# Optimization experiments

Measured on AMD Instinct MI355X. Metric: run time of the kernel, lower is better.

Reference implementation:

```python
import jax, jax.numpy as jnp
import numpy as np

H_BANDWIDTH = 0.5
EPS = 1e-5


def setup_inputs() -> dict:
    key = jax.random.key(0)
    k1, k2 = jax.random.split(key)
    x = jax.random.normal(k1, (4, 256, 64, 64), dtype=jnp.float32)
    y = jax.random.normal(k2, (4, 256, 64, 64), dtype=jnp.float32)
    return {"x": x, "y": y}


def reference(x, y):
    # x, y: (N, C, H, W), H=W=64 so no pooling branch is taken
    N, C, H, W = x.shape
    # mean over batch and spatial dims of y -> per-channel mu, shape (1, C, 1, 1)
    y_mu = jnp.mean(y, axis=(0, 2, 3)).reshape(1, C, 1, 1)
    x_c = x - y_mu
    y_c = y - y_mu
    # L2-normalize over channel dim
    x_n = x_c / jnp.linalg.norm(x_c, axis=1, keepdims=True)
    y_n = y_c / jnp.linalg.norm(y_c, axis=1, keepdims=True)
    x_n = x_n.reshape(N, C, H * W)
    y_n = y_n.reshape(N, C, H * W)
    # cosine similarity: (N, HW, HW)
    cos = jnp.einsum("ncp,ncq->npq", x_n, y_n)
    d = 1.0 - cos
    d_min = jnp.min(d, axis=2, keepdims=True)
    d_tilde = d / (d_min + EPS)
    w = jnp.exp((1.0 - d_tilde) / H_BANDWIDTH)
    cx_ij = w / jnp.sum(w, axis=2, keepdims=True)
    cx = jnp.mean(jnp.max(cx_ij, axis=1), axis=1)  # (N,)
    cx_loss = jnp.mean(-jnp.log(cx + EPS))
    return cx_loss
```

## Files before the change

### kernel.cpp

```cpp
#include <hip/hip_runtime.h>
#include <hip/hip_bf16.h>

typedef short bf16x8 __attribute__((ext_vector_type(8)));
typedef float f32x4 __attribute__((ext_vector_type(4)));

#define NB 4
#define C 256
#define HW 4096
#define NROWS (NB * HW)
#define EPSF 1e-5f

__device__ __forceinline__ unsigned short f2bf(float f) {
    unsigned int u = __float_as_uint(f);
    unsigned int r = u + 0x7fffu + ((u >> 16) & 1u);
    return (unsigned short)(r >> 16);
}
__device__ __forceinline__ float bf2f(unsigned int h) {
    return __uint_as_float(h << 16);
}
__device__ __forceinline__ void unpack8(uint4 u, float* v) {
    unsigned int w0 = u.x, w1 = u.y, w2 = u.z, w3 = u.w;
    v[0] = bf2f(w0 & 0xffffu); v[1] = bf2f(w0 >> 16);
    v[2] = bf2f(w1 & 0xffffu); v[3] = bf2f(w1 >> 16);
    v[4] = bf2f(w2 & 0xffffu); v[5] = bf2f(w2 >> 16);
    v[6] = bf2f(w3 & 0xffffu); v[7] = bf2f(w3 >> 16);
}
__device__ __forceinline__ float waveReduceSum(float v) {
    for (int off = 32; off > 0; off >>= 1) v += __shfl_xor(v, off);
    return v;
}
typedef __attribute__((address_space(1))) const unsigned int glb_cu;
typedef __attribute__((address_space(3))) unsigned int lds_u;
__device__ __forceinline__ void async_copy16(const unsigned short* g, unsigned short* l) {
    __builtin_amdgcn_global_load_lds((glb_cu*)g, (lds_u*)l, 16, 0, 0);
}

__global__ __launch_bounds__(256) void mu_kernel(const float* __restrict__ y,
                                                 float* __restrict__ mu,
                                                 float* __restrict__ cxsum,
                                                 unsigned int* __restrict__ ticket) {
    int c = blockIdx.x;
    int tid = threadIdx.x;
    if (c == 0) {
        if (tid < NB) cxsum[tid] = 0.f;
        if (tid == NB) *ticket = 0u;
    }
    float s = 0.f;
    const float* base = y + (size_t)c * HW;
    for (int n = 0; n < NB; n++) {
        const float* bn = base + (size_t)n * C * HW;
        for (int i = tid; i < HW; i += 256) s += bn[i];
    }
    s = waveReduceSum(s);
    __shared__ float red[4];
    int lane = tid & 63, wave = tid >> 6;
    if (lane == 0) red[wave] = s;
    __syncthreads();
    if (tid == 0) mu[c] = (red[0] + red[1] + red[2] + red[3]) * (1.0f / 16384.0f);
}

#define TP 32
#define TSTRIDE 257
__global__ __launch_bounds__(256) void prep_kernel(const float* __restrict__ x,
                                                   const float* __restrict__ y,
                                                   const float* __restrict__ mu,
                                                   unsigned short* __restrict__ Xn,
                                                   unsigned short* __restrict__ Yn) {
    __shared__ float smu[C];
    __shared__ float tile[TP * TSTRIDE];
    __shared__ float red[8 * 32];
    __shared__ float invn[TP];
    int tid = threadIdx.x;
    smu[tid] = mu[tid];
    int blk = blockIdx.x;
    int n = blk >> 7;
    int p0 = (blk & 127) * TP;
    int tp = tid & 31, cc = tid >> 5;
    __syncthreads();
    for (int pass = 0; pass < 2; pass++) {
        const float* in = pass ? y : x;
        unsigned short* out = pass ? Yn : Xn;
        const float* base = in + (size_t)n * C * HW + p0 + tp;
        float ssq = 0.f;
        for (int c = cc; c < C; c += 8) {
            float v = base[(size_t)c * HW] - smu[c];
            tile[tp * TSTRIDE + c] = v;
            ssq += v * v;
        }
        red[cc * 32 + tp] = ssq;
        __syncthreads();
        if (tid < 32) {
            float s = 0.f;
            for (int k = 0; k < 8; k++) s += red[k * 32 + tid];
            invn[tid] = rsqrtf(s);
        }
        __syncthreads();
        int c2 = (tid & 127) * 2;
        int pp = tid >> 7;
        for (int p = pp; p < TP; p += 2) {
            float inv = invn[p];
            unsigned short b0 = f2bf(tile[p * TSTRIDE + c2] * inv);
            unsigned short b1 = f2bf(tile[p * TSTRIDE + c2 + 1] * inv);
            unsigned int pack = (unsigned int)b0 | ((unsigned int)b1 << 16);
            ((unsigned int*)out)[(size_t)(n * HW + p0 + p) * (C / 2) + (c2 >> 1)] = pack;
        }
        __syncthreads();
    }
}

#define EPSTRIDE 136
#define STAGE(s)                                                               \
    do {                                                                       \
        unsigned short* lA = lds_us;                                           \
        unsigned short* lB = lds_us + 8192;                                    \
        _Pragma("unroll")                                                      \
        for (int t = 0; t < 4; t++) {                                          \
            int slot = t * 256 + tid;                                          \
            int r = slot >> 3, cl = slot & 7;                                  \
            int c = (s) * 8 + (cl ^ (r & 7));                                  \
            async_copy16(Ab + (size_t)r * C + c * 8, lA + slot * 8);           \
        }                                                                      \
        _Pragma("unroll")                                                      \
        for (int t = 0; t < 4; t++) {                                          \
            int slot = t * 256 + tid;                                          \
            int r = slot >> 3, cl = slot & 7;                                  \
            int c = (s) * 8 + (cl ^ (r & 7));                                  \
            async_copy16(Bb + (size_t)r * C + c * 8, lB + slot * 8);           \
        }                                                                      \
    } while (0)

#define COMPUTE()                                                              \
    do {                                                                       \
        const unsigned short* lA = lds_us;                                     \
        const unsigned short* lB = lds_us + 8192;                              \
        _Pragma("unroll")                                                      \
        for (int kkl = 0; kkl < 2; kkl++) {                                    \
            int cl4 = kkl * 4 + quad;                                          \
            int clp = cl4 ^ (mrow & 7);                                        \
            bf16x8 af[4], bfr[4];                                              \
            _Pragma("unroll")                                                  \
            for (int i = 0; i < 4; i++) {                                      \
                af[i]  = *(const bf16x8*)(lA + (wm + i * 16 + mrow) * 64 + clp * 8); \
                bfr[i] = *(const bf16x8*)(lB + (wn + i * 16 + mrow) * 64 + clp * 8); \
            }                                                                  \
            _Pragma("unroll")                                                  \
            for (int i = 0; i < 4; i++)                                        \
                _Pragma("unroll")                                              \
                for (int j = 0; j < 4; j++)                                    \
                    acc[i][j] = __builtin_amdgcn_mfma_f32_16x16x32_bf16(af[i], bfr[j], acc[i][j], 0, 0, 0); \
        }                                                                      \
    } while (0)

__global__ __launch_bounds__(256, 4) void gemm_cos(const unsigned short* __restrict__ Xn,
                                                   const unsigned short* __restrict__ Yn,
                                                   unsigned short* __restrict__ Cos) {
    __shared__ unsigned short lds_us[17408];
    int n = blockIdx.z;
    int pBase = blockIdx.y * 128, qBase = blockIdx.x * 128;
    const unsigned short* Ab = Xn + ((size_t)n * HW + pBase) * C;
    const unsigned short* Bb = Yn + ((size_t)n * HW + qBase) * C;
    int tid = threadIdx.x, lane = tid & 63, wave = tid >> 6;
    int wm = (wave >> 1) * 64, wn = (wave & 1) * 64;
    int mrow = lane & 15, quad = lane >> 4;

    f32x4 acc[4][4];
#pragma unroll
    for (int i = 0; i < 4; i++)
#pragma unroll
        for (int j = 0; j < 4; j++) acc[i][j] = (f32x4){0.f, 0.f, 0.f, 0.f};

#pragma unroll
    for (int s = 0; s < 4; s++) {
        STAGE(s);
        __syncthreads();
        COMPUTE();
        __syncthreads();
    }

    unsigned short* epb = lds_us;
    int col = lane & 15, quad4 = quad * 4;
#pragma unroll
    for (int i = 0; i < 4; i++)
#pragma unroll
        for (int j = 0; j < 4; j++)
#pragma unroll
            for (int r = 0; r < 4; r++)
                epb[(wm + i * 16 + quad4 + r) * EPSTRIDE + wn + j * 16 + col] = f2bf(acc[i][j][r]);
    __syncthreads();
    unsigned short* Crow = Cos + (size_t)n * HW * HW;
#pragma unroll
    for (int it = 0; it < 8; it++) {
        int e = it * 2048 + tid * 8;
        int r = e >> 7, cg = e & 127;
        uint4 o = *(const uint4*)(epb + r * EPSTRIDE + cg);
        *(uint4*)(Crow + (size_t)(pBase + r) * HW + qBase + cg) = o;
    }
}

__global__ __launch_bounds__(256, 3) void rowcol(const unsigned short* __restrict__ Cos,
                                                 unsigned short* __restrict__ partial) {
    int n = blockIdx.y, chunk = blockIdx.x;
    int tid = threadIdx.x, lane = tid & 63, wave = tid >> 6;
    const unsigned short* rowbase = Cos + ((size_t)n * HW + chunk * 8) * HW;
    __shared__ float redm[8][4];
    __shared__ float sval[8][4];

    uint4 d[8][2];
#pragma unroll
    for (int r = 0; r < 8; r++) {
        const unsigned short* rp = rowbase + (size_t)r * HW;
        d[r][0] = *(const uint4*)(rp + tid * 8);
        d[r][1] = *(const uint4*)(rp + 2048 + tid * 8);
    }

    float m8[8];
#pragma unroll
    for (int r = 0; r < 8; r++) {
        float v[16];
        unpack8(d[r][0], v); unpack8(d[r][1], v + 8);
        float m = v[0];
#pragma unroll
        for (int k = 1; k < 16; k++) m = fmaxf(m, v[k]);
        m8[r] = m;
    }
#pragma unroll
    for (int off = 32; off > 0; off >>= 1)
#pragma unroll
        for (int r = 0; r < 8; r++) m8[r] = fmaxf(m8[r], __shfl_xor(m8[r], off));
    if (lane == 0)
#pragma unroll
        for (int r = 0; r < 8; r++) redm[r][wave] = m8[r];
    __syncthreads();

    float alpha[8], basec[8];
#pragma unroll
    for (int r = 0; r < 8; r++) {
        float M = fmaxf(fmaxf(redm[r][0], redm[r][1]), fmaxf(redm[r][2], redm[r][3]));
        alpha[r] = 2.0f / ((1.0f - M) + EPSF);
        basec[r] = 2.0f - alpha[r];
    }

    float s8[8];
#pragma unroll
    for (int r = 0; r < 8; r++) {
        float v[16];
        unpack8(d[r][0], v); unpack8(d[r][1], v + 8);
        float s = 0.f;
#pragma unroll
        for (int k = 0; k < 16; k++) s += __expf(fmaf(alpha[r], v[k], basec[r]));
        s8[r] = s;
    }
#pragma unroll
    for (int off = 32; off > 0; off >>= 1)
#pragma unroll
        for (int r = 0; r < 8; r++) s8[r] += __shfl_xor(s8[r], off);
    if (lane == 0)
#pragma unroll
        for (int r = 0; r < 8; r++) sval[r][wave] = s8[r];
    __syncthreads();

    float cmax[16];
#pragma unroll
    for (int k = 0; k < 16; k++) cmax[k] = -1e30f;
#pragma unroll
    for (int r = 0; r < 8; r++) {
        float S = sval[r][0] + sval[r][1] + sval[r][2] + sval[r][3];
        float beta = basec[r] - __logf(S);
        float v[16];
        unpack8(d[r][0], v); unpack8(d[r][1], v + 8);
#pragma unroll
        for (int k = 0; k < 16; k++) cmax[k] = fmaxf(cmax[k], fmaf(alpha[r], v[k], beta));
    }

    unsigned short* outp = partial + ((size_t)(n * 512 + chunk)) * HW;
    uint4 o0, o1;
    o0.x = (unsigned int)f2bf(cmax[0]) | ((unsigned int)f2bf(cmax[1]) << 16);
    o0.y = (unsigned int)f2bf(cmax[2]) | ((unsigned int)f2bf(cmax[3]) << 16);
    o0.z = (unsigned int)f2bf(cmax[4]) | ((unsigned int)f2bf(cmax[5]) << 16);
    o0.w = (unsigned int)f2bf(cmax[6]) | ((unsigned int)f2bf(cmax[7]) << 16);
    o1.x = (unsigned int)f2bf(cmax[8]) | ((unsigned int)f2bf(cmax[9]) << 16);
    o1.y = (unsigned int)f2bf(cmax[10]) | ((unsigned int)f2bf(cmax[11]) << 16);
    o1.z = (unsigned int)f2bf(cmax[12]) | ((unsigned int)f2bf(cmax[13]) << 16);
    o1.w = (unsigned int)f2bf(cmax[14]) | ((unsigned int)f2bf(cmax[15]) << 16);
    *(uint4*)(outp + tid * 8) = o0;
    *(uint4*)(outp + 2048 + tid * 8) = o1;
}

__global__ __launch_bounds__(256) void colred(const unsigned short* __restrict__ partial,
                                              float* __restrict__ cxsum,
                                              unsigned int* __restrict__ ticket,
                                              float* __restrict__ out) {
    int n = blockIdx.y, g = blockIdx.x;
    int tid = threadIdx.x;
    int qo = tid & 7;
    int cs = tid >> 3;
    const unsigned short* p = partial + ((size_t)(n * 512 + cs)) * HW + g * 64 + qo * 8;
    float mx[8];
#pragma unroll
    for (int k = 0; k < 8; k++) mx[k] = -1e30f;
#pragma unroll 4
    for (int c = cs; c < 512; c += 32) {
        uint4 u = *(const uint4*)p;
        float v[8];
        unpack8(u, v);
#pragma unroll
        for (int k = 0; k < 8; k++) mx[k] = fmaxf(mx[k], v[k]);
        p += (size_t)32 * HW;
    }
    __shared__ float sm[32][64];
#pragma unroll
    for (int k = 0; k < 8; k++) sm[cs][qo * 8 + k] = mx[k];
    __syncthreads();
    if (tid < 64) {
        float mm = -1e30f;
#pragma unroll
        for (int s = 0; s < 32; s++) mm = fmaxf(mm, sm[s][tid]);
        float sv = __expf(mm);
        sv = waveReduceSum(sv);
        if (tid == 0) {
            atomicAdd(&cxsum[n], sv);
            __threadfence();
            unsigned int old = atomicAdd(ticket, 1u);
            if (old == (unsigned int)(64 * NB - 1)) {
                __threadfence();
                float loss = 0.f;
                for (int b = 0; b < NB; b++) {
                    float csn = atomicAdd(&cxsum[b], 0.0f);
                    loss += -logf(csn * (1.0f / 4096.0f) + EPSF);
                }
                out[0] = loss * 0.25f;
            }
        }
    }
}

extern "C" void kernel_launch(void* const* d_in, const int* in_sizes, int n_in,
                              void* d_out, int out_size, void* d_ws, size_t ws_size,
                              hipStream_t stream) {
    const float* x = (const float*)d_in[0];
    const float* y = (const float*)d_in[1];
    float* out = (float*)d_out;
    char* ws = (char*)d_ws;

    float* mu               = (float*)(ws + 0);
    float* cxsum            = (float*)(ws + 1024);
    unsigned int* ticket    = (unsigned int*)(ws + 1040);
    unsigned short* Xn      = (unsigned short*)(ws + 2097152);
    unsigned short* Yn      = (unsigned short*)(ws + 10485760);
    unsigned short* partial = (unsigned short*)(ws + 2097152);
    unsigned short* Cos     = (unsigned short*)(ws + 18874368);

    mu_kernel<<<C, 256, 0, stream>>>(y, mu, cxsum, ticket);
    prep_kernel<<<NROWS / TP, 256, 0, stream>>>(x, y, mu, Xn, Yn);
    gemm_cos<<<dim3(HW / 128, HW / 128, NB), 256, 0, stream>>>(Xn, Yn, Cos);
    rowcol<<<dim3(512, NB), 256, 0, stream>>>(Cos, partial);
    colred<<<dim3(64, NB), 256, 0, stream>>>(partial, cxsum, ticket, out);
}
```

Baseline: 197.0 us.

## Widen parallelism and vectorize loads in mu, prep and column-reduce kernels

The mu kernel now runs one block per (channel, batch) pair, reading with float4 loads and writing per-batch partial sums that prep_kernel combines. prep_kernel loads four spatial positions per thread with float4 instead of scalar loads, and the sum-of-squares reduction grows to 32 partials. colred launches twice as many blocks, each covering 32 columns over 64 row-slices, with the ticket threshold adjusted to match. The aim is more blocks in flight and fewer, wider memory transactions in the memory-bound auxiliary kernels, at the cost of extra partial-sum traffic and scattered LDS stores in the prep transpose.

Result: faster. 172.9 us (-12.2%).

```diff
diff --git a/kernel.cpp b/kernel.cpp
--- a/kernel.cpp
+++ b/kernel.cpp
@@ -36,62 +36,73 @@
 }
 
 __global__ __launch_bounds__(256) void mu_kernel(const float* __restrict__ y,
-                                                 float* __restrict__ mu,
+                                                 float* __restrict__ mup,
                                                  float* __restrict__ cxsum,
                                                  unsigned int* __restrict__ ticket) {
-    int c = blockIdx.x;
+    int c = blockIdx.x, n = blockIdx.y;
     int tid = threadIdx.x;
-    if (c == 0) {
+    if (c == 0 && n == 0) {
         if (tid < NB) cxsum[tid] = 0.f;
         if (tid == NB) *ticket = 0u;
     }
+    const float4* b4 = (const float4*)(y + (size_t)n * C * HW + (size_t)c * HW);
     float s = 0.f;
-    const float* base = y + (size_t)c * HW;
-    for (int n = 0; n < NB; n++) {
-        const float* bn = base + (size_t)n * C * HW;
-        for (int i = tid; i < HW; i += 256) s += bn[i];
+#pragma unroll
+    for (int k = 0; k < 4; k++) {
+        float4 v = b4[tid + k * 256];
+        s += (v.x + v.y) + (v.z + v.w);
     }
     s = waveReduceSum(s);
     __shared__ float red[4];
     int lane = tid & 63, wave = tid >> 6;
     if (lane == 0) red[wave] = s;
     __syncthreads();
-    if (tid == 0) mu[c] = (red[0] + red[1] + red[2] + red[3]) * (1.0f / 16384.0f);
+    if (tid == 0) mup[n * C + c] = (red[0] + red[1]) + (red[2] + red[3]);
 }
 
 #define TP 32
 #define TSTRIDE 257
 __global__ __launch_bounds__(256) void prep_kernel(const float* __restrict__ x,
                                                    const float* __restrict__ y,
-                                                   const float* __restrict__ mu,
+                                                   const float* __restrict__ mup,
                                                    unsigned short* __restrict__ Xn,
                                                    unsigned short* __restrict__ Yn) {
     __shared__ float smu[C];
     __shared__ float tile[TP * TSTRIDE];
-    __shared__ float red[8 * 32];
+    __shared__ float red[32 * 32];
     __shared__ float invn[TP];
     int tid = threadIdx.x;
-    smu[tid] = mu[tid];
+    smu[tid] = (mup[tid] + mup[C + tid] + mup[2 * C + tid] + mup[3 * C + tid]) * (1.0f / 16384.0f);
     int blk = blockIdx.x;
     int n = blk >> 7;
     int p0 = (blk & 127) * TP;
-    int tp = tid & 31, cc = tid >> 5;
+    int tq = tid & 7;
+    int cc = tid >> 3;
     __syncthreads();
     for (int pass = 0; pass < 2; pass++) {
         const float* in = pass ? y : x;
         unsigned short* out = pass ? Yn : Xn;
-        const float* base = in + (size_t)n * C * HW + p0 + tp;
-        float ssq = 0.f;
-        for (int c = cc; c < C; c += 8) {
-            float v = base[(size_t)c * HW] - smu[c];
-            tile[tp * TSTRIDE + c] = v;
-            ssq += v * v;
+        const float* base = in + (size_t)n * C * HW + p0 + tq * 4;
+        float ssq0 = 0.f, ssq1 = 0.f, ssq2 = 0.f, ssq3 = 0.f;
+        for (int c = cc; c < C; c += 32) {
+            float4 v = *(const float4*)(base + (size_t)c * HW);
+            float m = smu[c];
+            v.x -= m; v.y -= m; v.z -= m; v.w -= m;
+            tile[(tq * 4 + 0) * TSTRIDE + c] = v.x;
+            tile[(tq * 4 + 1) * TSTRIDE + c] = v.y;
+            tile[(tq * 4 + 2) * TSTRIDE + c] = v.z;
+            tile[(tq * 4 + 3) * TSTRIDE + c] = v.w;
+            ssq0 += v.x * v.x; ssq1 += v.y * v.y;
+            ssq2 += v.z * v.z; ssq3 += v.w * v.w;
         }
-        red[cc * 32 + tp] = ssq;
+        red[cc * 32 + tq * 4 + 0] = ssq0;
+        red[cc * 32 + tq * 4 + 1] = ssq1;
+        red[cc * 32 + tq * 4 + 2] = ssq2;
+        red[cc * 32 + tq * 4 + 3] = ssq3;
         __syncthreads();
         if (tid < 32) {
             float s = 0.f;
-            for (int k = 0; k < 8; k++) s += red[k * 32 + tid];
+            for (int k = 0; k < 32; k++) s += red[k * 32 + tid];
             invn[tid] = rsqrtf(s);
         }
         __syncthreads();
@@ -292,36 +303,37 @@
                                               float* __restrict__ out) {
     int n = blockIdx.y, g = blockIdx.x;
     int tid = threadIdx.x;
-    int qo = tid & 7;
-    int cs = tid >> 3;
-    const unsigned short* p = partial + ((size_t)(n * 512 + cs)) * HW + g * 64 + qo * 8;
+    int qo = tid & 3;
+    int cs = tid >> 2;
+    const unsigned short* p = partial + ((size_t)(n * 512 + cs)) * HW + g * 32 + qo * 8;
     float mx[8];
 #pragma unroll
     for (int k = 0; k < 8; k++) mx[k] = -1e30f;
 #pragma unroll 4
-    for (int c = cs; c < 512; c += 32) {
+    for (int c = cs; c < 512; c += 64) {
         uint4 u = *(const uint4*)p;
         float v[8];
         unpack8(u, v);
 #pragma unroll
         for (int k = 0; k < 8; k++) mx[k] = fmaxf(mx[k], v[k]);
-        p += (size_t)32 * HW;
-    }
-    __shared__ float sm[32][64];
+        p += (size_t)64 * HW;
+    }
+    __shared__ float sm[64][32];
 #pragma unroll
     for (int k = 0; k < 8; k++) sm[cs][qo * 8 + k] = mx[k];
     __syncthreads();
-    if (tid < 64) {
+    if (tid < 32) {
         float mm = -1e30f;
 #pragma unroll
-        for (int s = 0; s < 32; s++) mm = fmaxf(mm, sm[s][tid]);
+        for (int s = 0; s < 64; s++) mm = fmaxf(mm, sm[s][tid]);
         float sv = __expf(mm);
-        sv = waveReduceSum(sv);
+#pragma unroll
+        for (int off = 16; off > 0; off >>= 1) sv += __shfl_xor(sv, off);
         if (tid == 0) {
             atomicAdd(&cxsum[n], sv);
             __threadfence();
             unsigned int old = atomicAdd(ticket, 1u);
-            if (old == (unsigned int)(64 * NB - 1)) {
+            if (old == (unsigned int)(128 * NB - 1)) {
                 __threadfence();
                 float loss = 0.f;
                 for (int b = 0; b < NB; b++) {
@@ -342,17 +354,17 @@
     float* out = (float*)d_out;
     char* ws = (char*)d_ws;
 
-    float* mu               = (float*)(ws + 0);
-    float* cxsum            = (float*)(ws + 1024);
-    unsigned int* ticket    = (unsigned int*)(ws + 1040);
+    float* mup              = (float*)(ws + 0);
+    float* cxsum            = (float*)(ws + 8192);
+    unsigned int* ticket    = (unsigned int*)(ws + 8208);
     unsigned short* Xn      = (unsigned short*)(ws + 2097152);
     unsigned short* Yn      = (unsigned short*)(ws + 10485760);
     unsigned short* partial = (unsigned short*)(ws + 2097152);
     unsigned short* Cos     = (unsigned short*)(ws + 18874368);
 
-    mu_kernel<<<C, 256, 0, stream>>>(y, mu, cxsum, ticket);
-    prep_kernel<<<NROWS / TP, 256, 0, stream>>>(x, y, mu, Xn, Yn);
+    mu_kernel<<<dim3(C, NB), 256, 0, stream>>>(y, mup, cxsum, ticket);
+    prep_kernel<<<NROWS / TP, 256, 0, stream>>>(x, y, mup, Xn, Yn);
     gemm_cos<<<dim3(HW / 128, HW / 128, NB), 256, 0, stream>>>(Xn, Yn, Cos);
     rowcol<<<dim3(512, NB), 256, 0, stream>>>(Cos, partial);
-    colred<<<dim3(64, NB), 256, 0, stream>>>(partial, cxsum, ticket, out);
-}
+    colred<<<dim3(128, NB), 256, 0, stream>>>(partial, cxsum, ticket, out);
+}
```
